# Performance work log

Measured on AMD Instinct MI355X. Metric: run time of the kernel, lower is better.

The kernel has to match this reference:

```python
import jax, jax.numpy as jnp
import numpy as np

NH = 8      # num_head
WIN = 7     # window
EPS = 1e-6


def _ln(x, w, b):
    m = x.mean(-1, keepdims=True)
    v = ((x - m) ** 2).mean(-1, keepdims=True)
    return (x - m) / jnp.sqrt(v + EPS) * w + b


def _dwconv(x, w, b):
    # x: [B,H,W,Cc], w: [7,7,1,Cc] (HWIO), depthwise (groups=Cc)
    y = jax.lax.conv_general_dilated(
        x, w, window_strides=(1, 1), padding='SAME',
        dimension_numbers=('NHWC', 'HWIO', 'NHWC'),
        feature_group_count=x.shape[-1])
    return y + b


def setup_inputs() -> dict:
    B, H, W, C = 16, 56, 56, 256
    RATIO = 8
    key = jax.random.key(0)
    ki = iter(jax.random.split(key, 48))
    def lin(i, o):
        return jax.random.normal(next(ki), (i, o), jnp.float32) * (1.0 / i) ** 0.5
    def bias(o):
        return jnp.zeros((o,), jnp.float32)
    def dw(c):
        return jax.random.normal(next(ki), (7, 7, 1, c), jnp.float32) * 0.05
    inp = {
        'x':   jax.random.normal(next(ki), (B, H, W, C), jnp.float32),
        'x_e': jax.random.normal(next(ki), (B, H, W, C // 2), jnp.float32),
        # LayerNorms
        'norm_w': jnp.ones((C,), jnp.float32),  'norm_b': bias(C),
        'norme_w': jnp.ones((C // 2,), jnp.float32), 'norme_b': bias(C // 2),
        # local_rr path
        'rr1_w': lin(C, C), 'rr1_b': bias(C),
        'rr2_w': lin(C, C), 'rr2_b': bias(C),
        'rr3_w': lin(C, C), 'rr3_b': bias(C),
        'conv_w': dw(C), 'conv_b': bias(C),
        # LocalAttentionRGBT
        'lx_l1_w': lin(C, C // 2), 'lx_l1_b': bias(C // 2),
        'lx_l2_w': lin(C // 2, C // 2), 'lx_l2_b': bias(C // 2),
        'lx_c1_w': dw(C // 2), 'lx_c1_b': bias(C // 2),
        'lx_c2_w': dw(C // 2), 'lx_c2_b': bias(C // 2),
        'lx_fc1_w': lin(C, C // RATIO),  # no bias
        'lx_fc2_w': lin(C // RATIO, C),  # no bias
        'lx_l3_w': lin(C, C // 2), 'lx_l3_b': bias(C // 2),
        # global pooled attention
        'kv_w': lin(C, C), 'kv_b': bias(C),
        'q_w': lin(C // 2 * 3, C // 2), 'q_b': bias(C // 2),
        # output projections (window != 0 => in = 2C)
        'proj_w': lin(2 * C, C), 'proj_b': bias(C),
        'proje_w': lin(2 * C, C // 2), 'proje_b': bias(C // 2),
    }
    return inp


def reference(x, x_e, norm_w, norm_b, norme_w, norme_b,
              rr1_w, rr1_b, rr2_w, rr2_b, rr3_w, rr3_b, conv_w, conv_b,
              lx_l1_w, lx_l1_b, lx_l2_w, lx_l2_b, lx_c1_w, lx_c1_b,
              lx_c2_w, lx_c2_b, lx_fc1_w, lx_fc2_w, lx_l3_w, lx_l3_b,
              kv_w, kv_b, q_w, q_b, proj_w, proj_b, proje_w, proje_b):
    B, H, W, C = x.shape
    hd = C // NH // 2  # head dim
    x = _ln(x, norm_w, norm_b)
    x_e = _ln(x_e, norme_w, norme_b)

    # --- local_rr: gated depthwise-conv branch ---
    rr1 = x @ rr1_w + rr1_b
    rr2 = _dwconv(x @ rr2_w + rr2_b, conv_w, conv_b)
    rr2 = rr2 @ rr3_w + rr3_b
    local_rr = rr1 * rr2  # [B,H,W,C]

    # --- LocalAttentionRGBT: cross-modal cosine-sim channel gate ---
    rgb = x @ lx_l1_w + lx_l1_b      # [B,H,W,C/2]
    t = x_e @ lx_l2_w + lx_l2_b      # [B,H,W,C/2]
    co = _dwconv(rgb * t, lx_c1_w, lx_c1_b)
    di = _dwconv(jnp.abs(rgb - t), lx_c2_w, lx_c2_b)
    co_di = jnp.concatenate([co, di], axis=-1)           # [B,H,W,C]
    amap = co_di.mean(-1, keepdims=True)                 # [B,H,W,1]
    dot = (amap * co_di).sum((1, 2), keepdims=True)      # [B,1,1,C]
    n1 = jnp.sqrt((amap ** 2).sum((1, 2), keepdims=True))
    n2 = jnp.sqrt((co_di ** 2).sum((1, 2), keepdims=True))
    cos_sim = dot / (n1 * n2 + 1e-6)                     # [B,1,1,C]
    attn_c = jax.nn.sigmoid(
        jax.nn.gelu(cos_sim @ lx_fc1_w, approximate=False) @ lx_fc2_w)
    local_rx = (co_di * attn_c) @ lx_l3_w + lx_l3_b      # [B,H,W,C/2]

    # --- global: pooled-q full-kv attention ---
    kv = (x @ kv_w + kv_b).reshape(B, H * W, 2, NH, hd).transpose(2, 0, 3, 1, 4)
    k, v = kv[0], kv[1]                                  # [B,NH,HW,hd]
    rx = jnp.concatenate([x, x_e], axis=-1)              # [B,H,W,3C/2]
    rx_pool = rx.reshape(B, WIN, H // WIN, WIN, W // WIN, -1).mean((2, 4))  # [B,7,7,3C/2]
    q = (rx_pool @ q_w + q_b).reshape(B, WIN * WIN, NH, hd).transpose(0, 2, 1, 3)
    scores = jnp.einsum('bnqd,bnkd->bnqk', q * hd ** -0.5, k)  # [B,NH,49,HW]
    attn = jax.nn.softmax(scores, axis=-1)
    g = jnp.einsum('bnqk,bnkd->bnqd', attn, v)           # [B,NH,49,hd]
    g = g.reshape(B, NH, WIN, WIN, hd).transpose(0, 1, 4, 2, 3).reshape(B, C // 2, WIN, WIN)
    g = jax.image.resize(g, (B, C // 2, H, W), method='bilinear')  # align_corners=False
    g = g.transpose(0, 2, 3, 1)                          # [B,H,W,C/2]

    cat = jnp.concatenate([local_rr, local_rx, g], axis=-1)  # [B,H,W,2C]
    x_e_out = cat @ proje_w + proje_b
    x_out = cat @ proj_w + proj_b
    return (x_out, x_e_out)
```

## Files before the change

kernel.cpp:

```cpp
#include <hip/hip_runtime.h>
#include <hip/hip_bf16.h>
#include <cstdint>
#include <cstddef>

#define N_TOK 50176
#define HWSZ  3136
#define BATCH 16

#define GF_MUL     1
#define GF_ASCALE  2
#define GF_KVSPLIT 4

typedef __hip_bfloat16 bf16;
typedef __attribute__((ext_vector_type(8))) short bf16x8;
typedef __attribute__((ext_vector_type(4))) float f32x4;
typedef __attribute__((ext_vector_type(4))) unsigned short u16x4;

__device__ __forceinline__ void  stf(float* p, size_t i, float v) { p[i] = v; }
__device__ __forceinline__ void  stf(bf16* p, size_t i, float v) { p[i] = __float2bfloat16(v); }
__device__ __forceinline__ float bu2f(unsigned short u) {
    unsigned int x = ((unsigned int)u) << 16; float f; __builtin_memcpy(&f, &x, 4); return f;
}
__device__ __forceinline__ unsigned short f2bu(float f) {
    bf16 t = __float2bfloat16(f); unsigned short u; __builtin_memcpy(&u, &t, 2); return u;
}

struct WtrDesc { const float* src; bf16* dst; int K; int N; int off; };
struct WtrPack { WtrDesc d[9]; int total; };
__global__ __launch_bounds__(256) void wtr_all(WtrPack p)
{
    int idx = blockIdx.x * 256 + threadIdx.x;
    if (idx >= p.total) return;
    #pragma unroll
    for (int s = 0; s < 9; s++) {
        int lo = p.d[s].off, hi = lo + p.d[s].K * p.d[s].N;
        if (idx >= lo && idx < hi) {
            int j = idx - lo;
            int k = j / p.d[s].N, n = j % p.d[s].N;
            p.d[s].dst[(size_t)n * p.d[s].K + k] = __float2bfloat16(p.d[s].src[j]);
        }
    }
}

__global__ __launch_bounds__(256) void ln_kernel(const float* __restrict__ in,
    const float* __restrict__ w, const float* __restrict__ b,
    bf16* __restrict__ out, int rows, int Cdim)
{
    int wave = threadIdx.x >> 6, lane = threadIdx.x & 63;
    int row = blockIdx.x * 4 + wave;
    if (row >= rows) return;
    const float* p = in + (size_t)row * Cdim;
    int nj = Cdim >> 6;
    float v[4];
    float s = 0.f;
    for (int j = 0; j < nj; j++) { v[j] = p[lane + 64 * j]; s += v[j]; }
    for (int off = 32; off; off >>= 1) s += __shfl_xor(s, off, 64);
    float mean = s / (float)Cdim;
    float vs = 0.f;
    for (int j = 0; j < nj; j++) { float d = v[j] - mean; vs += d * d; }
    for (int off = 32; off; off >>= 1) vs += __shfl_xor(vs, off, 64);
    float rstd = 1.f / sqrtf(vs / (float)Cdim + 1e-6f);
    bf16* q = out + (size_t)row * Cdim;
    for (int j = 0; j < nj; j++) {
        int c = lane + 64 * j;
        q[c] = __float2bfloat16((v[j] - mean) * rstd * w[c] + b[c]);
    }
}

#define LDT 56
template<int FLAGS, typename OT>
__global__ __launch_bounds__(256) void gemm_mfma(
    const bf16* __restrict__ A, int lda,
    const bf16* __restrict__ WT,
    const float* __restrict__ bias,
    OT* __restrict__ C, int ldc,
    int M, int K, int N,
    const bf16* __restrict__ mul, int mulld,
    const float* __restrict__ ascale,
    bf16* __restrict__ kout, bf16* __restrict__ vout)
{
    __shared__ bf16 As[128][LDT];
    __shared__ bf16 Bs[128][LDT];
    int ntile = N >> 7;
    int m0 = (blockIdx.x / ntile) * 128;
    int n0 = (blockIdx.x % ntile) * 128;
    int tid = threadIdx.x;
    int lane = tid & 63, wid = tid >> 6;
    int wr = (wid >> 1) * 64, wc = (wid & 1) * 64;
    int lrow = lane & 15, lko = (lane >> 4) * 8;

    f32x4 acc[4][4];
    #pragma unroll
    for (int i = 0; i < 4; i++)
        #pragma unroll
        for (int j = 0; j < 4; j++)
            acc[i][j] = (f32x4){0.f, 0.f, 0.f, 0.f};

    for (int k0 = 0; k0 < K; k0 += 32) {
        #pragma unroll
        for (int i = 0; i < 2; i++) {
            int idx = tid + i * 256;
            int r = idx >> 2, ko = (idx & 3) * 8;
            bf16x8 v = *reinterpret_cast<const bf16x8*>(A + (size_t)(m0 + r) * lda + k0 + ko);
            if (FLAGS & GF_ASCALE) {
                int bidx = (m0 + r) / HWSZ;
                const float* as = ascale + (size_t)bidx * K + k0 + ko;
                #pragma unroll
                for (int e = 0; e < 8; e++)
                    v[e] = (short)f2bu(bu2f((unsigned short)v[e]) * as[e]);
            }
            *reinterpret_cast<bf16x8*>(&As[r][ko]) = v;
            bf16x8 wv = *reinterpret_cast<const bf16x8*>(WT + (size_t)(n0 + r) * K + k0 + ko);
            *reinterpret_cast<bf16x8*>(&Bs[r][ko]) = wv;
        }
        __syncthreads();
        bf16x8 af[4], br[4];
        #pragma unroll
        for (int i = 0; i < 4; i++)
            af[i] = *reinterpret_cast<const bf16x8*>(&As[wr + i * 16 + lrow][lko]);
        #pragma unroll
        for (int j = 0; j < 4; j++)
            br[j] = *reinterpret_cast<const bf16x8*>(&Bs[wc + j * 16 + lrow][lko]);
        #pragma unroll
        for (int i = 0; i < 4; i++)
            #pragma unroll
            for (int j = 0; j < 4; j++)
                acc[i][j] = __builtin_amdgcn_mfma_f32_16x16x32_bf16(af[i], br[j], acc[i][j], 0, 0, 0);
        __syncthreads();
    }

    int orow = (lane >> 4) * 4;
    int ocol = lane & 15;
    #pragma unroll
    for (int i = 0; i < 4; i++) {
        #pragma unroll
        for (int j = 0; j < 4; j++) {
            #pragma unroll
            for (int p = 0; p < 4; p++) {
                int gm = m0 + wr + i * 16 + orow + p;
                int gn = n0 + wc + j * 16 + ocol;
                float v = acc[i][j][p] + bias[gn];
                if (FLAGS & GF_KVSPLIT) {
                    int bb = gm / HWSZ, n = gm % HWSZ;
                    if (gn < 128)
                        kout[(((size_t)bb * 8 + (gn >> 4)) * HWSZ + n) * 16 + (gn & 15)] = __float2bfloat16(v);
                    else {
                        int hh = (gn - 128) >> 4, dd = (gn - 128) & 15;
                        vout[(((size_t)bb * 8 + hh) * 16 + dd) * HWSZ + n] = __float2bfloat16(v);
                    }
                } else {
                    if (FLAGS & GF_MUL) v *= __bfloat162float(mul[(size_t)gm * mulld + gn]);
                    stf(C, (size_t)gm * ldc + gn, v);
                }
            }
        }
    }
}

__global__ __launch_bounds__(256) void gemm_k(
    const float* __restrict__ A, int lda,
    const float* __restrict__ Wt, const float* __restrict__ bias,
    float* __restrict__ Cc, int ldc, int M, int K, int Nc)
{
    __shared__ float As[16][68];
    __shared__ float Ws[16][64];
    int ntile = Nc >> 6;
    int tile_n = blockIdx.x % ntile;
    int tile_m = blockIdx.x / ntile;
    int m0 = tile_m * 64, n0 = tile_n * 64;
    int tid = threadIdx.x;
    int tx = tid & 15, ty = tid >> 4;
    float acc[4][4] = {};
    for (int k0 = 0; k0 < K; k0 += 16) {
        int ks = tid & 15, ms = tid >> 4;
        #pragma unroll
        for (int i = 0; i < 4; i++) {
            int gm = m0 + ms + i * 16;
            As[ks][ms + i * 16] = (gm < M) ? A[(size_t)gm * lda + k0 + ks] : 0.f;
        }
        #pragma unroll
        for (int j = 0; j < 4; j++) {
            int k = (tid >> 6) * 4 + j;
            Ws[k][tid & 63] = Wt[(size_t)(k0 + k) * Nc + n0 + (tid & 63)];
        }
        __syncthreads();
        #pragma unroll
        for (int k = 0; k < 16; k++) {
            float a[4], w[4];
            #pragma unroll
            for (int i = 0; i < 4; i++) a[i] = As[k][ty * 4 + i];
            #pragma unroll
            for (int j = 0; j < 4; j++) w[j] = Ws[k][tx * 4 + j];
            #pragma unroll
            for (int i = 0; i < 4; i++)
                #pragma unroll
                for (int j = 0; j < 4; j++)
                    acc[i][j] += a[i] * w[j];
        }
        __syncthreads();
    }
    #pragma unroll
    for (int i = 0; i < 4; i++) {
        int gm = m0 + ty * 4 + i;
        if (gm >= M) continue;
        #pragma unroll
        for (int j = 0; j < 4; j++) {
            int gn = n0 + tx * 4 + j;
            Cc[(size_t)gm * ldc + gn] = acc[i][j] + bias[gn];
        }
    }
}

__global__ __launch_bounds__(256) void dwconv_reg(const bf16* __restrict__ in,
    bf16* __restrict__ out,
    const float* __restrict__ w0, const float* __restrict__ b0,
    const float* __restrict__ w1, const float* __restrict__ b1, int split)
{
    int tid = threadIdx.x;
    int chg = tid & 31;
    int bsw = (blockIdx.x & 7) * 196 + (blockIdx.x >> 3);
    int pg  = bsw * 8 + (tid >> 5);
    int xg = pg % 14;
    int y  = (pg / 14) % 56;
    int b  = pg / (14 * 56);
    int c0 = chg * 8;
    int x0 = xg * 4;

    const float* wp; const float* bp; int ws, cw;
    if (c0 < split) { wp = w0; bp = b0; ws = split;       cw = c0; }
    else            { wp = w1; bp = b1; ws = 256 - split; cw = c0 - split; }

    float acc[4][8];
    #pragma unroll
    for (int o = 0; o < 4; o++)
        #pragma unroll
        for (int e = 0; e < 8; e++) acc[o][e] = 0.f;

    const bf16* base = in + (size_t)b * HWSZ * 256 + c0;
    const float* wbase = wp + cw;
    #pragma unroll
    for (int ky = 0; ky < 7; ky++) {
        int gy = y + ky - 3;
        if (gy < 0 || gy >= 56) continue;
        const bf16* rowp = base + (size_t)gy * 56 * 256;
        float cf[10][8];
        #pragma unroll
        for (int j = 0; j < 10; j++) {
            int gx = x0 + j - 3;
            bf16x8 v = {0, 0, 0, 0, 0, 0, 0, 0};
            if ((unsigned)gx < 56u)
                v = *reinterpret_cast<const bf16x8*>(rowp + (size_t)gx * 256);
            #pragma unroll
            for (int e = 0; e < 8; e++) cf[j][e] = bu2f((unsigned short)v[e]);
        }
        const float* wrow = wbase + ky * 7 * ws;
        #pragma unroll
        for (int kx = 0; kx < 7; kx++) {
            float4 wa = *reinterpret_cast<const float4*>(wrow + kx * ws);
            float4 wb = *reinterpret_cast<const float4*>(wrow + kx * ws + 4);
            #pragma unroll
            for (int o = 0; o < 4; o++) {
                acc[o][0] += cf[o + kx][0] * wa.x;
                acc[o][1] += cf[o + kx][1] * wa.y;
                acc[o][2] += cf[o + kx][2] * wa.z;
                acc[o][3] += cf[o + kx][3] * wa.w;
                acc[o][4] += cf[o + kx][4] * wb.x;
                acc[o][5] += cf[o + kx][5] * wb.y;
                acc[o][6] += cf[o + kx][6] * wb.z;
                acc[o][7] += cf[o + kx][7] * wb.w;
            }
        }
    }

    float4 ba = *reinterpret_cast<const float4*>(bp + cw);
    float4 bb = *reinterpret_cast<const float4*>(bp + cw + 4);
    bf16* obase = out + (((size_t)b * HWSZ + (size_t)y * 56 + x0) * 256) + c0;
    #pragma unroll
    for (int o = 0; o < 4; o++) {
        bf16x8 ov;
        ov[0] = (short)f2bu(acc[o][0] + ba.x);
        ov[1] = (short)f2bu(acc[o][1] + ba.y);
        ov[2] = (short)f2bu(acc[o][2] + ba.z);
        ov[3] = (short)f2bu(acc[o][3] + ba.w);
        ov[4] = (short)f2bu(acc[o][4] + bb.x);
        ov[5] = (short)f2bu(acc[o][5] + bb.y);
        ov[6] = (short)f2bu(acc[o][6] + bb.z);
        ov[7] = (short)f2bu(acc[o][7] + bb.w);
        *reinterpret_cast<bf16x8*>(obase + (size_t)o * 256) = ov;
    }
}

__global__ void rgbt_k(const bf16* __restrict__ rgb, const bf16* __restrict__ t,
                       bf16* __restrict__ codin, int total )
{
    int i = blockIdx.x * blockDim.x + threadIdx.x;
    if (i >= total) return;
    int n = i >> 7, c = i & 127;
    float a = __bfloat162float(rgb[i]), bb = __bfloat162float(t[i]);
    codin[(size_t)n * 256 + c] = __float2bfloat16(a * bb);
    codin[(size_t)n * 256 + 128 + c] = __float2bfloat16(fabsf(a - bb));
}

__global__ __launch_bounds__(256) void cosred_k(const bf16* __restrict__ codi,
    float* __restrict__ part)
{
    int b = blockIdx.x >> 4;
    int bi = blockIdx.x & 15;
    int wave = threadIdx.x >> 6, lane = threadIdx.x & 63;
    int slot = bi * 4 + wave;
    float dloc[4] = {0,0,0,0}, n2loc[4] = {0,0,0,0};
    float n1loc = 0.f;
    for (int i = 0; i < 49; i++) {
        int p = slot * 49 + i;
        const bf16* row = codi + ((size_t)b * HWSZ + p) * 256;
        float v[4]; float sum = 0.f;
        #pragma unroll
        for (int j = 0; j < 4; j++) { v[j] = __bfloat162float(row[lane + 64 * j]); sum += v[j]; }
        for (int off = 32; off; off >>= 1) sum += __shfl_xor(sum, off, 64);
        float amap = sum * (1.f / 256.f);
        #pragma unroll
        for (int j = 0; j < 4; j++) { dloc[j] += amap * v[j]; n2loc[j] += v[j] * v[j]; }
        n1loc += amap * amap;
    }
    float* dst = part + ((size_t)b * 64 + slot) * 513;
    #pragma unroll
    for (int j = 0; j < 4; j++) {
        dst[lane + 64 * j] = dloc[j];
        dst[256 + lane + 64 * j] = n2loc[j];
    }
    if (lane == 0) dst[512] = n1loc;
}

__global__ __launch_bounds__(256) void mlp_kernel(const float* __restrict__ part,
    const float* __restrict__ fc1w, const float* __restrict__ fc2w,
    float* __restrict__ attnc)
{
    int b = blockIdx.x;
    int tid = threadIdx.x;
    __shared__ float cosb[256];
    __shared__ float hbuf[32];
    const float* pb = part + (size_t)b * 64 * 513;
    float dot = 0.f, n2 = 0.f, n1 = 0.f;
    for (int s = 0; s < 64; s++) {
        dot += pb[s * 513 + tid];
        n2  += pb[s * 513 + 256 + tid];
        n1  += pb[s * 513 + 512];
    }
    float cs = dot / (sqrtf(n1) * sqrtf(n2) + 1e-6f);
    cosb[tid] = cs;
    __syncthreads();
    if (tid < 32) {
        float h = 0.f;
        for (int c = 0; c < 256; c++) h += cosb[c] * fc1w[c * 32 + tid];
        h = 0.5f * h * (1.f + erff(h * 0.70710678f));
        hbuf[tid] = h;
    }
    __syncthreads();
    float o = 0.f;
    for (int j = 0; j < 32; j++) o += hbuf[j] * fc2w[j * 256 + tid];
    attnc[b * 256 + tid] = 1.f / (1.f + expf(-o));
}

__global__ __launch_bounds__(384) void pool_kernel(const bf16* __restrict__ xn,
    const bf16* __restrict__ xen, float* __restrict__ rxpool)
{
    int bij = blockIdx.x;
    int b = bij / 49; int ij = bij % 49; int i = ij / 7, j = ij % 7;
    int c = threadIdx.x;
    float s = 0.f;
    for (int dy = 0; dy < 8; dy++)
        for (int dx = 0; dx < 8; dx++) {
            size_t n = ((size_t)b * 56 + (i * 8 + dy)) * 56 + (j * 8 + dx);
            s += (c < 256) ? __bfloat162float(xn[n * 256 + c])
                           : __bfloat162float(xen[n * 128 + (c - 256)]);
        }
    rxpool[(size_t)bij * 384 + c] = s * (1.f / 64.f);
}

#define NSPLIT 14
#define POSB   224
__global__ __launch_bounds__(256) void attn_mfma(const float* __restrict__ qbuf,
    const bf16* __restrict__ kbuf, const bf16* __restrict__ vtbuf,
    float* __restrict__ osplit, float* __restrict__ mlbuf)
{
    int bh = blockIdx.x & 127;
    int split = blockIdx.x >> 7;
    int b = bh >> 3, h = bh & 7;
    int tid = threadIdx.x;
    int qt = tid >> 6;
    int lane = tid & 63;
    int lo = lane & 15, hi = lane >> 4;

    bf16x8 qf = {0, 0, 0, 0, 0, 0, 0, 0};
    int q = qt * 16 + lo;
    if (hi < 2 && q < 49) {
        const float* qp = qbuf + ((size_t)b * 49 + q) * 128 + h * 16 + hi * 8;
        #pragma unroll
        for (int j = 0; j < 8; j++) qf[j] = (short)f2bu(qp[j] * 0.25f);
    }
    const bf16* kbase = kbuf + (size_t)bh * HWSZ * 16;
    const bf16* vbase = vtbuf + ((size_t)bh * 16 + lo) * HWSZ;

    float m_run = -1e30f, l_run = 0.f;
    f32x4 oacc = {0.f, 0.f, 0.f, 0.f};
    int pos1 = 8 * (lo >> 2) + (lo & 3);
    const f32x4 zz = {0.f, 0.f, 0.f, 0.f};

    for (int t = 0; t < POSB / 32; t++) {
        int base = split * POSB + t * 32;
        bf16x8 kf1 = {0, 0, 0, 0, 0, 0, 0, 0}, kf2 = kf1;
        if (hi < 2) {
            kf1 = *reinterpret_cast<const bf16x8*>(kbase + (size_t)(base + pos1) * 16 + hi * 8);
            kf2 = *reinterpret_cast<const bf16x8*>(kbase + (size_t)(base + pos1 + 4) * 16 + hi * 8);
        }
        bf16x8 vf = *reinterpret_cast<const bf16x8*>(vbase + base + hi * 8);
        f32x4 s1 = __builtin_amdgcn_mfma_f32_16x16x32_bf16(kf1, qf, zz, 0, 0, 0);
        f32x4 s2 = __builtin_amdgcn_mfma_f32_16x16x32_bf16(kf2, qf, zz, 0, 0, 0);
        float pmax = fmaxf(fmaxf(fmaxf(s1[0], s1[1]), fmaxf(s1[2], s1[3])),
                           fmaxf(fmaxf(s2[0], s2[1]), fmaxf(s2[2], s2[3])));
        pmax = fmaxf(pmax, __shfl_xor(pmax, 16, 64));
        pmax = fmaxf(pmax, __shfl_xor(pmax, 32, 64));
        float mnew = fmaxf(m_run, pmax);
        float esc = __expf(m_run - mnew);
        l_run *= esc;
        float e0 = __shfl(esc, 4 * hi + 0, 64);
        float e1 = __shfl(esc, 4 * hi + 1, 64);
        float e2 = __shfl(esc, 4 * hi + 2, 64);
        float e3 = __shfl(esc, 4 * hi + 3, 64);
        oacc[0] *= e0; oacc[1] *= e1; oacc[2] *= e2; oacc[3] *= e3;
        float p0 = __expf(s1[0] - mnew), p1 = __expf(s1[1] - mnew);
        float p2 = __expf(s1[2] - mnew), p3 = __expf(s1[3] - mnew);
        float p4 = __expf(s2[0] - mnew), p5 = __expf(s2[1] - mnew);
        float p6 = __expf(s2[2] - mnew), p7 = __expf(s2[3] - mnew);
        float rs = ((p0 + p1) + (p2 + p3)) + ((p4 + p5) + (p6 + p7));
        rs += __shfl_xor(rs, 16, 64);
        rs += __shfl_xor(rs, 32, 64);
        l_run += rs;
        m_run = mnew;
        bf16x8 pf;
        pf[0] = (short)f2bu(p0); pf[1] = (short)f2bu(p1);
        pf[2] = (short)f2bu(p2); pf[3] = (short)f2bu(p3);
        pf[4] = (short)f2bu(p4); pf[5] = (short)f2bu(p5);
        pf[6] = (short)f2bu(p6); pf[7] = (short)f2bu(p7);
        oacc = __builtin_amdgcn_mfma_f32_16x16x32_bf16(pf, vf, oacc, 0, 0, 0);
    }

    float* ob = osplit + ((size_t)bh * NSPLIT + split) * 64 * 16;
    #pragma unroll
    for (int r = 0; r < 4; r++) {
        int qq = qt * 16 + 4 * hi + r;
        ob[(size_t)qq * 16 + lo] = oacc[r];
    }
    if (hi == 0) {
        float* mlb = mlbuf + (((size_t)bh * NSPLIT + split) * 64 + qt * 16 + lo) * 2;
        mlb[0] = m_run; mlb[1] = l_run;
    }
}

__global__ __launch_bounds__(256) void attn_combine(const float* __restrict__ osplit,
    const float* __restrict__ mlbuf, float* __restrict__ gs)
{
    int idx = blockIdx.x * 256 + threadIdx.x;
    if (idx >= 128 * 49 * 16) return;
    int d = idx & 15;
    int pq = idx >> 4;
    int bh = pq / 49, q = pq % 49;
    float m[NSPLIT], l[NSPLIT];
    float M = -1e30f;
    #pragma unroll
    for (int s = 0; s < NSPLIT; s++) {
        const float* mlb = mlbuf + (((size_t)bh * NSPLIT + s) * 64 + q) * 2;
        m[s] = mlb[0]; l[s] = mlb[1];
        M = fmaxf(M, m[s]);
    }
    float L = 0.f, O = 0.f;
    #pragma unroll
    for (int s = 0; s < NSPLIT; s++) {
        float e = __expf(m[s] - M);
        L += l[s] * e;
        O += osplit[(((size_t)bh * NSPLIT + s) * 64 + q) * 16 + d] * e;
    }
    gs[(size_t)pq * 16 + d] = O / L;
}

__global__ void upsample_kernel(const float* __restrict__ gs, bf16* __restrict__ cat)
{
    int idx = blockIdx.x * blockDim.x + threadIdx.x;
    if (idx >= N_TOK * 128) return;
    int c = idx & 127;
    int pos = idx >> 7;
    int h = c >> 4, d = c & 15;
    int x = pos % 56;
    int y = (pos / 56) % 56;
    int b = pos / HWSZ;
    float sy = (y + 0.5f) * 0.125f - 0.5f;
    float sx = (x + 0.5f) * 0.125f - 0.5f;
    int y0f = (int)floorf(sy); float wy = sy - (float)y0f;
    int x0f = (int)floorf(sx); float wx = sx - (float)x0f;
    int y0 = max(0, min(6, y0f)), y1 = max(0, min(6, y0f + 1));
    int x0 = max(0, min(6, x0f)), x1 = max(0, min(6, x0f + 1));
    const float* g0 = gs + ((size_t)(b * 8 + h) * 49) * 16 + d;
    float v00 = g0[(y0 * 7 + x0) * 16], v01 = g0[(y0 * 7 + x1) * 16];
    float v10 = g0[(y1 * 7 + x0) * 16], v11 = g0[(y1 * 7 + x1) * 16];
    float v0 = v00 + (v01 - v00) * wx;
    float v1 = v10 + (v11 - v10) * wx;
    float v = v0 + (v1 - v0) * wy;
    cat[(size_t)pos * 512 + 384 + c] = __float2bfloat16(v);
}

extern "C" void kernel_launch(void* const* d_in, const int* in_sizes, int n_in,
                              void* d_out, int out_size, void* d_ws, size_t ws_size,
                              hipStream_t stream)
{
    const float* x      = (const float*)d_in[0];
    const float* x_e    = (const float*)d_in[1];
    const float* norm_w = (const float*)d_in[2];
    const float* norm_b = (const float*)d_in[3];
    const float* norme_w= (const float*)d_in[4];
    const float* norme_b= (const float*)d_in[5];
    const float* rr1_w  = (const float*)d_in[6];
    const float* rr1_b  = (const float*)d_in[7];
    const float* rr2_w  = (const float*)d_in[8];
    const float* rr2_b  = (const float*)d_in[9];
    const float* rr3_w  = (const float*)d_in[10];
    const float* rr3_b  = (const float*)d_in[11];
    const float* conv_w = (const float*)d_in[12];
    const float* conv_b = (const float*)d_in[13];
    const float* l1_w   = (const float*)d_in[14];
    const float* l1_b   = (const float*)d_in[15];
    const float* l2_w   = (const float*)d_in[16];
    const float* l2_b   = (const float*)d_in[17];
    const float* c1_w   = (const float*)d_in[18];
    const float* c1_b   = (const float*)d_in[19];
    const float* c2_w   = (const float*)d_in[20];
    const float* c2_b   = (const float*)d_in[21];
    const float* fc1_w  = (const float*)d_in[22];
    const float* fc2_w  = (const float*)d_in[23];
    const float* l3_w   = (const float*)d_in[24];
    const float* l3_b   = (const float*)d_in[25];
    const float* kv_w   = (const float*)d_in[26];
    const float* kv_b   = (const float*)d_in[27];
    const float* q_w    = (const float*)d_in[28];
    const float* q_b    = (const float*)d_in[29];
    const float* proj_w = (const float*)d_in[30];
    const float* proj_b = (const float*)d_in[31];
    const float* proje_w= (const float*)d_in[32];
    const float* proje_b= (const float*)d_in[33];

    float* part   = (float*)d_ws;
    float* attnc  = part   + (size_t)525312;
    float* gs     = attnc  + 4096;
    float* rxpool = gs     + 100352;
    float* qbuf   = rxpool + 301056;
    bf16* wt      = (bf16*)(qbuf + 100352);
    bf16* rr1_t  = wt;
    bf16* rr2_t  = rr1_t + 65536;
    bf16* rr3_t  = rr2_t + 65536;
    bf16* kv_t   = rr3_t + 65536;
    bf16* l1_t   = kv_t  + 65536;
    bf16* l2_t   = l1_t  + 32768;
    bf16* l3_t   = l2_t  + 16384;
    bf16* proj_t = l3_t  + 32768;
    bf16* proje_t= proj_t + 131072;
    bf16* xn     = proje_t + 65536;
    bf16* xen    = xn   + (size_t)N_TOK * 256;
    bf16* bufC   = xen  + (size_t)N_TOK * 128;
    bf16* bufD   = bufC + (size_t)N_TOK * 256;
    bf16* bufE   = bufD + (size_t)N_TOK * 256;
    bf16* cat    = bufE + (size_t)N_TOK * 256;
    size_t need = (size_t)((char*)(cat + (size_t)N_TOK * 512) - (char*)d_ws);
    if (ws_size < need) return;

    bf16* kbuf = bufC;
    bf16* vbuf = bufC + (size_t)N_TOK * 128;

    float* osplit = (float*)bufD;
    float* mlbuf  = osplit + (size_t)128 * NSPLIT * 64 * 16;

    float* xout  = (float*)d_out;
    float* xeout = xout + (size_t)N_TOK * 256;

    const int nthr = 256;
    auto mgrid = [](int M, int N) { return dim3((M / 128) * (N / 128)); };

    {
        WtrPack p;
        const float* srcs[9] = {rr1_w, rr2_w, rr3_w, kv_w, l1_w, l2_w, l3_w, proj_w, proje_w};
        bf16* dsts[9] = {rr1_t, rr2_t, rr3_t, kv_t, l1_t, l2_t, l3_t, proj_t, proje_t};
        int Ks[9] = {256, 256, 256, 256, 256, 128, 256, 512, 512};
        int Ns[9] = {256, 256, 256, 256, 128, 128, 128, 256, 128};
        int off = 0;
        for (int s = 0; s < 9; s++) {
            p.d[s] = {srcs[s], dsts[s], Ks[s], Ns[s], off};
            off += Ks[s] * Ns[s];
        }
        p.total = off;
        wtr_all<<<dim3((off + 255) / 256), dim3(256), 0, stream>>>(p);
    }

    ln_kernel<<<dim3(N_TOK / 4), dim3(nthr), 0, stream>>>(x, norm_w, norm_b, xn, N_TOK, 256);
    ln_kernel<<<dim3(N_TOK / 4), dim3(nthr), 0, stream>>>(x_e, norme_w, norme_b, xen, N_TOK, 128);

    gemm_mfma<0, bf16><<<mgrid(N_TOK, 256), dim3(nthr), 0, stream>>>(
        xn, 256, rr1_t, rr1_b, bufC, 256, N_TOK, 256, 256, nullptr, 0, nullptr, nullptr, nullptr);
    gemm_mfma<0, bf16><<<mgrid(N_TOK, 256), dim3(nthr), 0, stream>>>(
        xn, 256, rr2_t, rr2_b, bufD, 256, N_TOK, 256, 256, nullptr, 0, nullptr, nullptr, nullptr);
    dwconv_reg<<<dim3(N_TOK / 32), dim3(nthr), 0, stream>>>(
        bufD, bufE, conv_w, conv_b, conv_w, conv_b, 256);
    gemm_mfma<GF_MUL, bf16><<<mgrid(N_TOK, 256), dim3(nthr), 0, stream>>>(
        bufE, 256, rr3_t, rr3_b, cat, 512, N_TOK, 256, 256, bufC, 256, nullptr, nullptr, nullptr);

    gemm_mfma<0, bf16><<<mgrid(N_TOK, 128), dim3(nthr), 0, stream>>>(
        xn, 256, l1_t, l1_b, bufD, 128, N_TOK, 256, 128, nullptr, 0, nullptr, nullptr, nullptr);
    gemm_mfma<0, bf16><<<mgrid(N_TOK, 128), dim3(nthr), 0, stream>>>(
        xen, 128, l2_t, l2_b, bufD + (size_t)N_TOK * 128, 128, N_TOK, 128, 128, nullptr, 0, nullptr, nullptr, nullptr);
    rgbt_k<<<dim3((N_TOK * 128) / nthr), dim3(nthr), 0, stream>>>(
        bufD, bufD + (size_t)N_TOK * 128, bufC, N_TOK * 128);
    dwconv_reg<<<dim3(N_TOK / 32), dim3(nthr), 0, stream>>>(
        bufC, bufE, c1_w, c1_b, c2_w, c2_b, 128);
    cosred_k<<<dim3(BATCH * 16), dim3(nthr), 0, stream>>>(bufE, part);
    mlp_kernel<<<dim3(BATCH), dim3(nthr), 0, stream>>>(part, fc1_w, fc2_w, attnc);
    gemm_mfma<GF_ASCALE, bf16><<<mgrid(N_TOK, 128), dim3(nthr), 0, stream>>>(
        bufE, 256, l3_t, l3_b, cat + 256, 512, N_TOK, 256, 128, nullptr, 0, attnc, nullptr, nullptr);

    gemm_mfma<GF_KVSPLIT, bf16><<<mgrid(N_TOK, 256), dim3(nthr), 0, stream>>>(
        xn, 256, kv_t, kv_b, (bf16*)nullptr, 0, N_TOK, 256, 256, nullptr, 0, nullptr, kbuf, vbuf);
    pool_kernel<<<dim3(BATCH * 49), dim3(384), 0, stream>>>(xn, xen, rxpool);
    gemm_k<<<dim3(((784 + 63) / 64) * 2), dim3(nthr), 0, stream>>>(
        rxpool, 384, q_w, q_b, qbuf, 128, 784, 384, 128);
    attn_mfma<<<dim3(128 * NSPLIT), dim3(nthr), 0, stream>>>(qbuf, kbuf, vbuf, osplit, mlbuf);
    attn_combine<<<dim3(392), dim3(nthr), 0, stream>>>(osplit, mlbuf, gs);
    upsample_kernel<<<dim3((N_TOK * 128) / nthr), dim3(nthr), 0, stream>>>(gs, cat);

    gemm_mfma<0, float><<<mgrid(N_TOK, 256), dim3(nthr), 0, stream>>>(
        cat, 512, proj_t, proj_b, xout, 256, N_TOK, 512, 256, nullptr, 0, nullptr, nullptr, nullptr);
    gemm_mfma<0, float><<<mgrid(N_TOK, 128), dim3(nthr), 0, stream>>>(
        cat, 512, proje_t, proje_b, xeout, 128, N_TOK, 512, 128, nullptr, 0, nullptr, nullptr, nullptr);
}
```

Baseline: 478.3 us.

## Fuse paired GEMMs sharing an input and register-prefetch next K tile

Adds a dual-output mode to the MFMA GEMM so rr1/rr2 (both reading xn) and proj/proje (both reading cat) each run as one wider GEMM. The epilogue splits columns to two outputs with separate biases. This removes a second full read of the shared activation and one launch per pair. The GEMM main loop also now loads the next K-slice of A/W into registers while the MFMAs consume the current LDS tile, to hide global-load latency. The fusion assumes the two transposed weight matrices sit back to back in memory, and the prefetch costs extra registers.

```diff
diff --git a/kernel.cpp b/kernel.cpp
--- a/kernel.cpp
+++ b/kernel.cpp
@@ -10,6 +10,7 @@
 #define GF_MUL     1
 #define GF_ASCALE  2
 #define GF_KVSPLIT 4
+#define GF_DUAL    8
 
 typedef __hip_bfloat16 bf16;
 typedef __attribute__((ext_vector_type(8))) short bf16x8;
@@ -77,7 +78,8 @@
     int M, int K, int N,
     const bf16* __restrict__ mul, int mulld,
     const float* __restrict__ ascale,
-    bf16* __restrict__ kout, bf16* __restrict__ vout)
+    bf16* __restrict__ kout, bf16* __restrict__ vout,
+    OT* __restrict__ C2, int ldc2, const float* __restrict__ bias2, int N1)
 {
     __shared__ bf16 As[128][LDT];
     __shared__ bf16 Bs[128][LDT];
@@ -88,6 +90,7 @@
     int lane = tid & 63, wid = tid >> 6;
     int wr = (wid >> 1) * 64, wc = (wid & 1) * 64;
     int lrow = lane & 15, lko = (lane >> 4) * 8;
+    int sr = tid >> 2, sko = (tid & 3) * 8;
 
     f32x4 acc[4][4];
     #pragma unroll
@@ -96,24 +99,46 @@
         for (int j = 0; j < 4; j++)
             acc[i][j] = (f32x4){0.f, 0.f, 0.f, 0.f};
 
+    bf16x8 ra[2], rb[2];
+    #pragma unroll
+    for (int i = 0; i < 2; i++) {
+        int r = sr + i * 64;
+        bf16x8 v = *reinterpret_cast<const bf16x8*>(A + (size_t)(m0 + r) * lda + sko);
+        if (FLAGS & GF_ASCALE) {
+            int bidx = (m0 + r) / HWSZ;
+            const float* as = ascale + (size_t)bidx * K + sko;
+            #pragma unroll
+            for (int e = 0; e < 8; e++)
+                v[e] = (short)f2bu(bu2f((unsigned short)v[e]) * as[e]);
+        }
+        ra[i] = v;
+        rb[i] = *reinterpret_cast<const bf16x8*>(WT + (size_t)(n0 + r) * K + sko);
+    }
+
     for (int k0 = 0; k0 < K; k0 += 32) {
         #pragma unroll
         for (int i = 0; i < 2; i++) {
-            int idx = tid + i * 256;
-            int r = idx >> 2, ko = (idx & 3) * 8;
-            bf16x8 v = *reinterpret_cast<const bf16x8*>(A + (size_t)(m0 + r) * lda + k0 + ko);
-            if (FLAGS & GF_ASCALE) {
-                int bidx = (m0 + r) / HWSZ;
-                const float* as = ascale + (size_t)bidx * K + k0 + ko;
-                #pragma unroll
-                for (int e = 0; e < 8; e++)
-                    v[e] = (short)f2bu(bu2f((unsigned short)v[e]) * as[e]);
+            *reinterpret_cast<bf16x8*>(&As[sr + i * 64][sko]) = ra[i];
+            *reinterpret_cast<bf16x8*>(&Bs[sr + i * 64][sko]) = rb[i];
+        }
+        __syncthreads();
+        int kn = k0 + 32;
+        if (kn < K) {
+            #pragma unroll
+            for (int i = 0; i < 2; i++) {
+                int r = sr + i * 64;
+                bf16x8 v = *reinterpret_cast<const bf16x8*>(A + (size_t)(m0 + r) * lda + kn + sko);
+                if (FLAGS & GF_ASCALE) {
+                    int bidx = (m0 + r) / HWSZ;
+                    const float* as = ascale + (size_t)bidx * K + kn + sko;
+                    #pragma unroll
+                    for (int e = 0; e < 8; e++)
+                        v[e] = (short)f2bu(bu2f((unsigned short)v[e]) * as[e]);
+                }
+                ra[i] = v;
+                rb[i] = *reinterpret_cast<const bf16x8*>(WT + (size_t)(n0 + r) * K + kn + sko);
             }
-            *reinterpret_cast<bf16x8*>(&As[r][ko]) = v;
-            bf16x8 wv = *reinterpret_cast<const bf16x8*>(WT + (size_t)(n0 + r) * K + k0 + ko);
-            *reinterpret_cast<bf16x8*>(&Bs[r][ko]) = wv;
-        }
-        __syncthreads();
+        }
         bf16x8 af[4], br[4];
         #pragma unroll
         for (int i = 0; i < 4; i++)
@@ -139,8 +164,8 @@
             for (int p = 0; p < 4; p++) {
                 int gm = m0 + wr + i * 16 + orow + p;
                 int gn = n0 + wc + j * 16 + ocol;
-                float v = acc[i][j][p] + bias[gn];
                 if (FLAGS & GF_KVSPLIT) {
+                    float v = acc[i][j][p] + bias[gn];
                     int bb = gm / HWSZ, n = gm % HWSZ;
                     if (gn < 128)
                         kout[(((size_t)bb * 8 + (gn >> 4)) * HWSZ + n) * 16 + (gn & 15)] = __float2bfloat16(v);
@@ -148,7 +173,16 @@
                         int hh = (gn - 128) >> 4, dd = (gn - 128) & 15;
                         vout[(((size_t)bb * 8 + hh) * 16 + dd) * HWSZ + n] = __float2bfloat16(v);
                     }
+                } else if (FLAGS & GF_DUAL) {
+                    if (gn < N1) {
+                        float v = acc[i][j][p] + bias[gn];
+                        stf(C, (size_t)gm * ldc + gn, v);
+                    } else {
+                        float v = acc[i][j][p] + bias2[gn - N1];
+                        stf(C2, (size_t)gm * ldc2 + (gn - N1), v);
+                    }
                 } else {
+                    float v = acc[i][j][p] + bias[gn];
                     if (FLAGS & GF_MUL) v *= __bfloat162float(mul[(size_t)gm * mulld + gn]);
                     stf(C, (size_t)gm * ldc + gn, v);
                 }
@@ -601,19 +635,21 @@
     ln_kernel<<<dim3(N_TOK / 4), dim3(nthr), 0, stream>>>(x, norm_w, norm_b, xn, N_TOK, 256);
     ln_kernel<<<dim3(N_TOK / 4), dim3(nthr), 0, stream>>>(x_e, norme_w, norme_b, xen, N_TOK, 128);
 
-    gemm_mfma<0, bf16><<<mgrid(N_TOK, 256), dim3(nthr), 0, stream>>>(
-        xn, 256, rr1_t, rr1_b, bufC, 256, N_TOK, 256, 256, nullptr, 0, nullptr, nullptr, nullptr);
-    gemm_mfma<0, bf16><<<mgrid(N_TOK, 256), dim3(nthr), 0, stream>>>(
-        xn, 256, rr2_t, rr2_b, bufD, 256, N_TOK, 256, 256, nullptr, 0, nullptr, nullptr, nullptr);
+    gemm_mfma<GF_DUAL, bf16><<<mgrid(N_TOK, 512), dim3(nthr), 0, stream>>>(
+        xn, 256, rr1_t, rr1_b, bufC, 256, N_TOK, 256, 512, nullptr, 0, nullptr, nullptr, nullptr,
+        bufD, 256, rr2_b, 256);
     dwconv_reg<<<dim3(N_TOK / 32), dim3(nthr), 0, stream>>>(
         bufD, bufE, conv_w, conv_b, conv_w, conv_b, 256);
     gemm_mfma<GF_MUL, bf16><<<mgrid(N_TOK, 256), dim3(nthr), 0, stream>>>(
-        bufE, 256, rr3_t, rr3_b, cat, 512, N_TOK, 256, 256, bufC, 256, nullptr, nullptr, nullptr);
+        bufE, 256, rr3_t, rr3_b, cat, 512, N_TOK, 256, 256, bufC, 256, nullptr, nullptr, nullptr,
+        nullptr, 0, nullptr, 0);
 
     gemm_mfma<0, bf16><<<mgrid(N_TOK, 128), dim3(nthr), 0, stream>>>(
-        xn, 256, l1_t, l1_b, bufD, 128, N_TOK, 256, 128, nullptr, 0, nullptr, nullptr, nullptr);
+        xn, 256, l1_t, l1_b, bufD, 128, N_TOK, 256, 128, nullptr, 0, nullptr, nullptr, nullptr,
+        nullptr, 0, nullptr, 0);
     gemm_mfma<0, bf16><<<mgrid(N_TOK, 128), dim3(nthr), 0, stream>>>(
-        xen, 128, l2_t, l2_b, bufD + (size_t)N_TOK * 128, 128, N_TOK, 128, 128, nullptr, 0, nullptr, nullptr, nullptr);
+        xen, 128, l2_t, l2_b, bufD + (size_t)N_TOK * 128, 128, N_TOK, 128, 128, nullptr, 0, nullptr, nullptr, nullptr,
+        nullptr, 0, nullptr, 0);
     rgbt_k<<<dim3((N_TOK * 128) / nthr), dim3(nthr), 0, stream>>>(
         bufD, bufD + (size_t)N_TOK * 128, bufC, N_TOK * 128);
     dwconv_reg<<<dim3(N_TOK / 32), dim3(nthr), 0, stream>>>(
@@ -621,10 +657,12 @@
     cosred_k<<<dim3(BATCH * 16), dim3(nthr), 0, stream>>>(bufE, part);
     mlp_kernel<<<dim3(BATCH), dim3(nthr), 0, stream>>>(part, fc1_w, fc2_w, attnc);
     gemm_mfma<GF_ASCALE, bf16><<<mgrid(N_TOK, 128), dim3(nthr), 0, stream>>>(
-        bufE, 256, l3_t, l3_b, cat + 256, 512, N_TOK, 256, 128, nullptr, 0, attnc, nullptr, nullptr);
+        bufE, 256, l3_t, l3_b, cat + 256, 512, N_TOK, 256, 128, nullptr, 0, attnc, nullptr, nullptr,
+        nullptr, 0, nullptr, 0);
 
     gemm_mfma<GF_KVSPLIT, bf16><<<mgrid(N_TOK, 256), dim3(nthr), 0, stream>>>(
-        xn, 256, kv_t, kv_b, (bf16*)nullptr, 0, N_TOK, 256, 256, nullptr, 0, nullptr, kbuf, vbuf);
+        xn, 256, kv_t, kv_b, (bf16*)nullptr, 0, N_TOK, 256, 256, nullptr, 0, nullptr, kbuf, vbuf,
+        nullptr, 0, nullptr, 0);
     pool_kernel<<<dim3(BATCH * 49), dim3(384), 0, stream>>>(xn, xen, rxpool);
     gemm_k<<<dim3(((784 + 63) / 64) * 2), dim3(nthr), 0, stream>>>(
         rxpool, 384, q_w, q_b, qbuf, 128, 784, 384, 128);
@@ -632,8 +670,7 @@
     attn_combine<<<dim3(392), dim3(nthr), 0, stream>>>(osplit, mlbuf, gs);
     upsample_kernel<<<dim3((N_TOK * 128) / nthr), dim3(nthr), 0, stream>>>(gs, cat);
 
-    gemm_mfma<0, float><<<mgrid(N_TOK, 256), dim3(nthr), 0, stream>>>(
-        cat, 512, proj_t, proj_b, xout, 256, N_TOK, 512, 256, nullptr, 0, nullptr, nullptr, nullptr);
-    gemm_mfma<0, float><<<mgrid(N_TOK, 128), dim3(nthr), 0, stream>>>(
-        cat, 512, proje_t, proje_b, xeout, 128, N_TOK, 512, 128, nullptr, 0, nullptr, nullptr, nullptr);
-}
+    gemm_mfma<GF_DUAL, float><<<mgrid(N_TOK, 384), dim3(nthr), 0, stream>>>(
+        cat, 512, proj_t, proj_b, xout, 256, N_TOK, 512, 384, nullptr, 0, nullptr, nullptr, nullptr,
+        xeout, 128, proje_b, 256);
+}
```

Result: faster. 451.2 us (-5.7%).
